# Kernel optimization log

Measured on AMD Instinct MI355X. Metric: run time of the kernel, lower is better.

The kernel has to match this reference:

```python
import jax, jax.numpy as jnp
import numpy as np

N_NODES = 50000
N_EDGES = 800000
IN_CH = 128
HEADS = 4
OUT_CH = 32  # heads * out = in (needed for residual add)


def setup_inputs() -> dict:
    key = jax.random.key(0)
    k1, k2, k3, k4, k5, k6 = jax.random.split(key, 6)
    x = jax.random.normal(k1, (N_NODES, IN_CH), dtype=jnp.float32)
    edge_index = jax.random.randint(k2, (2, N_EDGES), 0, N_NODES, dtype=jnp.int64)
    # GATConv params: lin weight [in, heads*out], attention vectors split src/dst, bias [heads*out]
    W = jax.random.normal(k3, (IN_CH, HEADS * OUT_CH), dtype=jnp.float32) * (1.0 / np.sqrt(IN_CH))
    a_src = jax.random.normal(k4, (HEADS, OUT_CH), dtype=jnp.float32) * 0.1
    a_dst = jax.random.normal(k5, (HEADS, OUT_CH), dtype=jnp.float32) * 0.1
    bias = jax.random.normal(k6, (HEADS * OUT_CH,), dtype=jnp.float32) * 0.01
    return {"x": x, "edge_index": edge_index, "W": W, "a_src": a_src, "a_dst": a_dst, "bias": bias}


def reference(x, edge_index, W, a_src, a_dst, bias):
    N = x.shape[0]
    H, C = a_src.shape
    # PyG GATConv default: add self loops (message flows src -> dst)
    loops = jnp.arange(N, dtype=edge_index.dtype)
    src = jnp.concatenate([edge_index[0], loops])
    dst = jnp.concatenate([edge_index[1], loops])

    h = (x @ W).reshape(N, H, C)                       # [N,H,C]
    alpha_s = jnp.einsum('nhc,hc->nh', h, a_src)       # [N,H]
    alpha_d = jnp.einsum('nhc,hc->nh', h, a_dst)       # [N,H]

    # per-edge logits, LeakyReLU(0.2)
    e = jax.nn.leaky_relu(alpha_s[src] + alpha_d[dst], negative_slope=0.2)  # [E,H]
    # segment softmax over incoming edges of each destination node
    m = jax.ops.segment_max(e, dst, num_segments=N)    # [N,H]
    p = jnp.exp(e - m[dst])
    denom = jax.ops.segment_sum(p, dst, num_segments=N)
    alpha = p / (denom[dst] + 1e-16)                   # [E,H]

    # weighted scatter-sum of source features
    msg = alpha[:, :, None] * h[src]                   # [E,H,C]
    out = jax.ops.segment_sum(msg, dst, num_segments=N)
    out = out.reshape(N, H * C) + bias                 # concat heads + bias

    return jax.nn.elu(out) + x                         # ELU + residual
```

## Files before the change

### kernel.cpp

```cpp
#include <hip/hip_runtime.h>
#include <math.h>


#define CH 128
#define BCOLS 144
#define BKT_SH 8
#define BKT_CAP 8192

typedef short bf16x8 __attribute__((ext_vector_type(8)));
typedef float f32x4 __attribute__((ext_vector_type(4)));

__device__ __forceinline__ short f2bf(float f) {
    unsigned int u = __builtin_bit_cast(unsigned int, f);
    u += 0x7FFFu + ((u >> 16) & 1u);
    return (short)(u >> 16);
}
__device__ __forceinline__ unsigned int cvtpk(float lo, float hi) {
    unsigned int r;
    asm("v_cvt_pk_bf16_f32 %0, %1, %2" : "=v"(r) : "v"(lo), "v"(hi));
    return r;
}
__device__ __forceinline__ float bflo(unsigned int u) {
    return __builtin_bit_cast(float, u << 16);
}
__device__ __forceinline__ float bfhi(unsigned int u) {
    return __builtin_bit_cast(float, u & 0xffff0000u);
}

__global__ void prep(const float* __restrict__ W, const float* __restrict__ a_src,
                     const float* __restrict__ a_dst, short* __restrict__ Wbf,
                     int* __restrict__ gcursor, int nbuk) {
    int i = blockIdx.x * 256 + threadIdx.x;
    if (i < CH * CH) {
        int k = i >> 7, n = i & 127;
        Wbf[n * CH + k] = f2bf(W[i]);
    }
    if (i < 2048) {
        int k = i & 127, idx = i >> 7;
        float sum = 0.f;
        if (idx < 8) {
            int h = idx & 3;
            const float* av = (idx < 4) ? a_src : a_dst;
            #pragma unroll
            for (int c = 0; c < 32; ++c) sum += W[k * CH + h * 32 + c] * av[h * 32 + c];
        }
        Wbf[(CH + idx) * CH + k] = f2bf(sum);
    }
    if (i < nbuk) gcursor[i] = i * BKT_CAP;
}

__device__ __forceinline__ void gemm_body(
    int bid, const float* __restrict__ x, const short* __restrict__ Wbf,
    unsigned short* __restrict__ hb, float* __restrict__ as_, float* __restrict__ ad_,
    int N, short* Wl)
{
    for (int v = threadIdx.x; v < BCOLS * 16; v += 256) {
        int n = v >> 4, k8 = v & 15;
        *(bf16x8*)&Wl[n * CH + ((k8 ^ (n & 7)) << 3)] = *(const bf16x8*)&Wbf[v * 8];
    }
    const int w = threadIdx.x >> 6, l = threadIdx.x & 63;
    const int lr = l & 15, lg = l >> 4;
    const int base = bid * 128 + w * 32;
    __syncthreads();

    bf16x8 afr[2][4];
    #pragma unroll
    for (int mt = 0; mt < 2; ++mt) {
        int arow = base + mt * 16 + lr;
        if (arow >= N) arow = N - 1;
        const float* xr = &x[(size_t)arow * CH + lg * 8];
        #pragma unroll
        for (int ks = 0; ks < 4; ++ks) {
            float4 p0 = *(const float4*)&xr[ks * 32];
            float4 p1 = *(const float4*)&xr[ks * 32 + 4];
            uint4 aw;
            aw.x = cvtpk(p0.x, p0.y); aw.y = cvtpk(p0.z, p0.w);
            aw.z = cvtpk(p1.x, p1.y); aw.w = cvtpk(p1.z, p1.w);
            afr[mt][ks] = __builtin_bit_cast(bf16x8, aw);
        }
    }

    f32x4 acc[2][9];
    #pragma unroll
    for (int mt = 0; mt < 2; ++mt)
        #pragma unroll
        for (int nt = 0; nt < 9; ++nt) acc[mt][nt] = (f32x4){0.f, 0.f, 0.f, 0.f};

    #pragma unroll
    for (int ks = 0; ks < 4; ++ks) {
        #pragma unroll
        for (int nt = 0; nt < 9; ++nt) {
            int col = nt * 16 + lr;
            bf16x8 bfr = *(const bf16x8*)&Wl[col * CH + (((ks * 4 + lg) ^ (col & 7)) << 3)];
            acc[0][nt] = __builtin_amdgcn_mfma_f32_16x16x32_bf16(afr[0][ks], bfr, acc[0][nt], 0, 0, 0);
            acc[1][nt] = __builtin_amdgcn_mfma_f32_16x16x32_bf16(afr[1][ks], bfr, acc[1][nt], 0, 0, 0);
        }
    }

    #pragma unroll
    for (int mt = 0; mt < 2; ++mt) {
        const int rbase = base + mt * 16 + lg * 4;
        #pragma unroll
        for (int nt = 0; nt < 8; ++nt) {
            #pragma unroll
            for (int r = 0; r < 4; r += 2) {
                unsigned int u = cvtpk(acc[mt][nt][r], acc[mt][nt][r + 1]);
                int orow = rbase + r;
                if (orow < N)     hb[(size_t)orow * CH + nt * 16 + lr] = (unsigned short)u;
                if (orow + 1 < N) hb[(size_t)(orow + 1) * CH + nt * 16 + lr] = (unsigned short)(u >> 16);
            }
        }
        #pragma unroll
        for (int r = 0; r < 4; ++r) {
            int orow = rbase + r;
            float val = acc[mt][8][r];
            if (orow < N) {
                if (lr < 4)      as_[orow * 4 + lr] = val;
                else if (lr < 8) ad_[orow * 4 + lr - 4] = val;
            }
        }
    }
}

__device__ __forceinline__ void scatter_body(
    int bid, const int* __restrict__ src, const int* __restrict__ dst,
    int* __restrict__ gcursor, int* __restrict__ ebuf, int E, int N, int NBUK,
    int* lh, int* gbase)
{
    const int t = threadIdx.x;
    for (int j = t; j < NBUK; j += 256) lh[j] = 0;
    __syncthreads();
    const int total = E + N;
    const int base = bid * 1024;
    int pv[4], bk[4], rk[4];
    #pragma unroll
    for (int k = 0; k < 4; ++k) {
        int i = base + k * 256 + t;
        if (i < total) {
            int s, d;
            if (i < E) { s = src[i]; d = dst[i]; }
            else       { s = i - E;  d = s; }
            bk[k] = d >> BKT_SH;
            pv[k] = s | ((d & 255) << 16);
            rk[k] = atomicAdd(&lh[bk[k]], 1);
        } else bk[k] = -1;
    }
    __syncthreads();
    for (int j = t; j < NBUK; j += 256)
        gbase[j] = lh[j] ? atomicAdd(&gcursor[j], lh[j]) : 0;
    __syncthreads();
    #pragma unroll
    for (int k = 0; k < 4; ++k)
        if (bk[k] >= 0) {
            int pos = gbase[bk[k]] + rk[k];
            if (pos < (bk[k] + 1) * BKT_CAP) ebuf[pos] = pv[k];
        }
}

__global__ __launch_bounds__(256) void gemm_scatter(
    const float* __restrict__ x, const short* __restrict__ Wbf,
    unsigned short* __restrict__ hb, float* __restrict__ as_, float* __restrict__ ad_,
    const int* __restrict__ src, const int* __restrict__ dst,
    int* __restrict__ gcursor, int* __restrict__ ebuf,
    int E, int N, int NBUK, int GB)
{
    __shared__ short Wl[BCOLS * CH];
    if ((int)blockIdx.x < GB) {
        gemm_body(blockIdx.x, x, Wbf, hb, as_, ad_, N, Wl);
    } else {
        int* lh = (int*)Wl;
        int* gbase = lh + 256;
        scatter_body(blockIdx.x - GB, src, dst, gcursor, ebuf, E, N, NBUK, lh, gbase);
    }
}

__global__ __launch_bounds__(256) void fine_scatter(
    const int* __restrict__ gcursor, int* __restrict__ ebuf,
    int* __restrict__ row_start, int* __restrict__ row_cnt, int N)
{
    __shared__ int st[BKT_CAP];
    __shared__ int lh[256], lofs[256], lcur[256];
    __shared__ int ws[4];
    const int b = blockIdx.x, t = threadIdx.x;
    const int p0 = b * BKT_CAP;
    int cnt = gcursor[b] - p0; if (cnt > BKT_CAP) cnt = BKT_CAP;
    const int nb = b << BKT_SH;
    lh[t] = 0; lcur[t] = 0;
    __syncthreads();
    for (int e = t; e < cnt; e += 256) {
        int v = ebuf[p0 + e];
        st[e] = v;
        atomicAdd(&lh[v >> 16], 1);
    }
    __syncthreads();
    int v = lh[t], s = v;
    const int lane = t & 63, w = t >> 6;
    #pragma unroll
    for (int off = 1; off < 64; off <<= 1) {
        int u = __shfl_up(s, off, 64);
        if (lane >= off) s += u;
    }
    if (lane == 63) ws[w] = s;
    __syncthreads();
    int wadd = 0;
    if (w > 0) wadd += ws[0];
    if (w > 1) wadd += ws[1];
    if (w > 2) wadd += ws[2];
    int ex = s - v + wadd;
    lofs[t] = ex;
    if (nb + t < N) { row_start[nb + t] = p0 + ex; row_cnt[nb + t] = v; }
    __syncthreads();
    for (int e = t; e < cnt; e += 256) {
        int pv = st[e];
        int ld = pv >> 16;
        int pos = p0 + lofs[ld] + atomicAdd(&lcur[ld], 1);
        ebuf[pos] = pv & 0xFFFF;
    }
}

#define PAIR4(PP, SS, IBASE)                                                    \
    {                                                                           \
        int b0 = 8 * (IBASE) + 4 * half;                                        \
        int b1 = b0 + 8, b2 = b0 + 16, b3 = b0 + 24;                            \
        float pb0 = __shfl((PP), b0 + h2, 64);                                  \
        float pb1 = __shfl((PP), b1 + h2, 64);                                  \
        float pb2 = __shfl((PP), b2 + h2, 64);                                  \
        float pb3 = __shfl((PP), b3 + h2, 64);                                  \
        int sb0 = __shfl((SS), b0, 64);                                         \
        int sb1 = __shfl((SS), b1, 64);                                         \
        int sb2 = __shfl((SS), b2, 64);                                         \
        int sb3 = __shfl((SS), b3, 64);                                         \
        uint2 hv0 = *(const uint2*)&hb[(size_t)sb0 * CH + l31 * 4];             \
        uint2 hv1 = *(const uint2*)&hb[(size_t)sb1 * CH + l31 * 4];             \
        uint2 hv2 = *(const uint2*)&hb[(size_t)sb2 * CH + l31 * 4];             \
        uint2 hv3 = *(const uint2*)&hb[(size_t)sb3 * CH + l31 * 4];             \
        acc0 = fmaf(pb0, bflo(hv0.x), acc0); acc1 = fmaf(pb0, bfhi(hv0.x), acc1); \
        acc2 = fmaf(pb0, bflo(hv0.y), acc2); acc3 = fmaf(pb0, bfhi(hv0.y), acc3); \
        acc0 = fmaf(pb1, bflo(hv1.x), acc0); acc1 = fmaf(pb1, bfhi(hv1.x), acc1); \
        acc2 = fmaf(pb1, bflo(hv1.y), acc2); acc3 = fmaf(pb1, bfhi(hv1.y), acc3); \
        acc0 = fmaf(pb2, bflo(hv2.x), acc0); acc1 = fmaf(pb2, bfhi(hv2.x), acc1); \
        acc2 = fmaf(pb2, bflo(hv2.y), acc2); acc3 = fmaf(pb2, bfhi(hv2.y), acc3); \
        acc0 = fmaf(pb3, bflo(hv3.x), acc0); acc1 = fmaf(pb3, bfhi(hv3.x), acc1); \
        acc2 = fmaf(pb3, bflo(hv3.y), acc2); acc3 = fmaf(pb3, bfhi(hv3.y), acc3); \
    }

#define PAIR1(PP, SS, IBASE)                                                    \
    {                                                                           \
        int b0 = 8 * (IBASE) + 4 * half;                                        \
        float pb0 = __shfl((PP), b0 + h2, 64);                                  \
        int   sb0 = __shfl((SS), b0, 64);                                       \
        uint2 hv0 = *(const uint2*)&hb[(size_t)sb0 * CH + l31 * 4];             \
        acc0 = fmaf(pb0, bflo(hv0.x), acc0); acc1 = fmaf(pb0, bfhi(hv0.x), acc1); \
        acc2 = fmaf(pb0, bflo(hv0.y), acc2); acc3 = fmaf(pb0, bfhi(hv0.y), acc3); \
    }

__global__ __launch_bounds__(256) void gat_aggregate(
    const unsigned short* __restrict__ hb, const float* __restrict__ as_,
    const float* __restrict__ ad_, const int* __restrict__ row_start,
    const int* __restrict__ row_cnt, const int* __restrict__ esrc,
    const float* __restrict__ bias, const float* __restrict__ x,
    float* __restrict__ out, int N)
{
    int wid = blockIdx.x * 4 + (threadIdx.x >> 6);
    int lane = threadIdx.x & 63;
    if (wid >= N) return;
    const int l31 = lane & 31;
    const int half = lane >> 5;
    const int hq = lane & 3;
    const int eslot = lane >> 2;
    const int h2 = l31 >> 3;
    const float adv = ad_[wid * 4 + hq];
    const int jb = row_start[wid];
    const int je = jb + row_cnt[wid];

    float denp = 0.f;
    float acc0 = 0.f, acc1 = 0.f, acc2 = 0.f, acc3 = 0.f;
    for (int j0 = jb; j0 < je; j0 += 32) {
        int ei0 = j0 + eslot, ei1 = j0 + 16 + eslot;
        int s0 = 0, s1 = 0; float p0 = 0.f, p1 = 0.f;
        if (ei0 < je) {
            s0 = esrc[ei0];
            float e = as_[s0 * 4 + hq] + adv;
            e = fmaxf(e, 0.2f * e);
            p0 = __expf(e);
        }
        if (ei1 < je) {
            s1 = esrc[ei1];
            float e = as_[s1 * 4 + hq] + adv;
            e = fmaxf(e, 0.2f * e);
            p1 = __expf(e);
        }
        denp += p0 + p1;
        int rem = je - j0; if (rem > 32) rem = 32;
        int npair = (rem + 1) >> 1;
        int npA = npair < 8 ? npair : 8;
        int i = 0;
        for (; i + 3 < npA; i += 4) PAIR4(p0, s0, i);
        for (; i < npA; ++i)        PAIR1(p0, s0, i);
        if (npair > 8) {
            int npB = npair - 8;
            i = 0;
            for (; i + 3 < npB; i += 4) PAIR4(p1, s1, i);
            for (; i < npB; ++i)        PAIR1(p1, s1, i);
        }
    }
    #pragma unroll
    for (int m = 4; m < 64; m <<= 1) denp += __shfl_xor(denp, m, 64);
    float den = __shfl(denp, h2, 64);
    acc0 += __shfl_xor(acc0, 32, 64);
    acc1 += __shfl_xor(acc1, 32, 64);
    acc2 += __shfl_xor(acc2, 32, 64);
    acc3 += __shfl_xor(acc3, 32, 64);
    if (half == 0) {
        float inv = 1.f / (den + 1e-16f);
        float4 bv = *(const float4*)&bias[l31 * 4];
        float4 xv = *(const float4*)&x[(size_t)wid * CH + l31 * 4];
        float o0 = acc0 * inv + bv.x;
        float o1 = acc1 * inv + bv.y;
        float o2 = acc2 * inv + bv.z;
        float o3 = acc3 * inv + bv.w;
        o0 = (o0 > 0.f) ? o0 : expm1f(o0);
        o1 = (o1 > 0.f) ? o1 : expm1f(o1);
        o2 = (o2 > 0.f) ? o2 : expm1f(o2);
        o3 = (o3 > 0.f) ? o3 : expm1f(o3);
        float4 ov = make_float4(o0 + xv.x, o1 + xv.y, o2 + xv.z, o3 + xv.w);
        *(float4*)&out[(size_t)wid * CH + l31 * 4] = ov;
    }
}

extern "C" void kernel_launch(void* const* d_in, const int* in_sizes, int n_in,
                              void* d_out, int out_size, void* d_ws, size_t ws_size,
                              hipStream_t stream) {
    const float* x     = (const float*)d_in[0];
    const int*   ei    = (const int*)d_in[1];
    const float* W     = (const float*)d_in[2];
    const float* a_src = (const float*)d_in[3];
    const float* a_dst = (const float*)d_in[4];
    const float* bias  = (const float*)d_in[5];
    float* out = (float*)d_out;

    const int N = in_sizes[0] / CH;
    const int E = in_sizes[1] / 2;
    const int* src = ei;
    const int* dst = ei + E;
    const int total = E + N;
    const int NBUK = (N + 255) >> BKT_SH;

    unsigned short* hb = (unsigned short*)d_ws;
    float* as_ = (float*)(hb + (size_t)N * CH);
    float* ad_ = as_ + (size_t)N * 4;
    short* Wbf = (short*)(ad_ + (size_t)N * 4);
    int* row_start = (int*)(Wbf + BCOLS * CH);
    int* row_cnt   = row_start + N;
    int* gcursor   = row_cnt + N;
    int* ebuf      = gcursor + 256;

    const int GB = (N + 127) / 128;
    const int SB = (total + 1023) / 1024;

    prep<<<64, 256, 0, stream>>>(W, a_src, a_dst, Wbf, gcursor, NBUK);
    gemm_scatter<<<GB + SB, 256, 0, stream>>>(x, Wbf, hb, as_, ad_,
                                              src, dst, gcursor, ebuf,
                                              E, N, NBUK, GB);
    fine_scatter<<<NBUK, 256, 0, stream>>>(gcursor, ebuf, row_start, row_cnt, N);
    gat_aggregate<<<(N + 3) / 4, 256, 0, stream>>>(hb, as_, ad_, row_start, row_cnt, ebuf, bias, x, out, N);
}
```

Baseline: 161.9 us.

## Fuse fine bucket sort into aggregation with 32-node buckets sorted in LDS

Shrinks the coarse scatter buckets from 256 to 32 destination nodes and removes the separate fine_scatter kernel. The aggregation kernel now loads each bucket, sorts it by destination in shared memory, and then has each wave aggregate 8 nodes, reading source ids from LDS instead of global ebuf. This drops a kernel launch, the global row_start/row_cnt arrays and a round trip of ebuf through memory. In exchange there are many more atomic buckets (about 1563) in the coarse scatter, and the bucket capacity of 768 could overflow for high-degree clusters, which would drop edges.

```diff
diff --git a/kernel.cpp b/kernel.cpp
--- a/kernel.cpp
+++ b/kernel.cpp
@@ -4,8 +4,10 @@
 
 #define CH 128
 #define BCOLS 144
-#define BKT_SH 8
-#define BKT_CAP 8192
+#define BKT_SH 5
+#define BKT_NODES 32
+#define BKT_CAP 768
+#define NBUK_PAD 1600
 
 typedef short bf16x8 __attribute__((ext_vector_type(8)));
 typedef float f32x4 __attribute__((ext_vector_type(4)));
@@ -141,7 +143,7 @@
             if (i < E) { s = src[i]; d = dst[i]; }
             else       { s = i - E;  d = s; }
             bk[k] = d >> BKT_SH;
-            pv[k] = s | ((d & 255) << 16);
+            pv[k] = s | ((d & (BKT_NODES - 1)) << 16);
             rk[k] = atomicAdd(&lh[bk[k]], 1);
         } else bk[k] = -1;
     }
@@ -169,52 +171,8 @@
         gemm_body(blockIdx.x, x, Wbf, hb, as_, ad_, N, Wl);
     } else {
         int* lh = (int*)Wl;
-        int* gbase = lh + 256;
+        int* gbase = lh + NBUK_PAD;
         scatter_body(blockIdx.x - GB, src, dst, gcursor, ebuf, E, N, NBUK, lh, gbase);
-    }
-}
-
-__global__ __launch_bounds__(256) void fine_scatter(
-    const int* __restrict__ gcursor, int* __restrict__ ebuf,
-    int* __restrict__ row_start, int* __restrict__ row_cnt, int N)
-{
-    __shared__ int st[BKT_CAP];
-    __shared__ int lh[256], lofs[256], lcur[256];
-    __shared__ int ws[4];
-    const int b = blockIdx.x, t = threadIdx.x;
-    const int p0 = b * BKT_CAP;
-    int cnt = gcursor[b] - p0; if (cnt > BKT_CAP) cnt = BKT_CAP;
-    const int nb = b << BKT_SH;
-    lh[t] = 0; lcur[t] = 0;
-    __syncthreads();
-    for (int e = t; e < cnt; e += 256) {
-        int v = ebuf[p0 + e];
-        st[e] = v;
-        atomicAdd(&lh[v >> 16], 1);
-    }
-    __syncthreads();
-    int v = lh[t], s = v;
-    const int lane = t & 63, w = t >> 6;
-    #pragma unroll
-    for (int off = 1; off < 64; off <<= 1) {
-        int u = __shfl_up(s, off, 64);
-        if (lane >= off) s += u;
-    }
-    if (lane == 63) ws[w] = s;
-    __syncthreads();
-    int wadd = 0;
-    if (w > 0) wadd += ws[0];
-    if (w > 1) wadd += ws[1];
-    if (w > 2) wadd += ws[2];
-    int ex = s - v + wadd;
-    lofs[t] = ex;
-    if (nb + t < N) { row_start[nb + t] = p0 + ex; row_cnt[nb + t] = v; }
-    __syncthreads();
-    for (int e = t; e < cnt; e += 256) {
-        int pv = st[e];
-        int ld = pv >> 16;
-        int pos = p0 + lofs[ld] + atomicAdd(&lcur[ld], 1);
-        ebuf[pos] = pv & 0xFFFF;
     }
 }
 
@@ -254,77 +212,113 @@
         acc2 = fmaf(pb0, bflo(hv0.y), acc2); acc3 = fmaf(pb0, bfhi(hv0.y), acc3); \
     }
 
-__global__ __launch_bounds__(256) void gat_aggregate(
+__global__ __launch_bounds__(256) void csr_aggregate(
+    const int* __restrict__ gcursor, const int* __restrict__ ebuf,
     const unsigned short* __restrict__ hb, const float* __restrict__ as_,
-    const float* __restrict__ ad_, const int* __restrict__ row_start,
-    const int* __restrict__ row_cnt, const int* __restrict__ esrc,
-    const float* __restrict__ bias, const float* __restrict__ x,
-    float* __restrict__ out, int N)
+    const float* __restrict__ ad_, const float* __restrict__ bias,
+    const float* __restrict__ x, float* __restrict__ out, int N)
 {
-    int wid = blockIdx.x * 4 + (threadIdx.x >> 6);
-    int lane = threadIdx.x & 63;
-    if (wid >= N) return;
+    __shared__ int st[BKT_CAP];
+    __shared__ unsigned short st2[BKT_CAP];
+    __shared__ int lh[BKT_NODES], lofs[BKT_NODES], lcur[BKT_NODES];
+    const int b = blockIdx.x, t = threadIdx.x;
+    const int p0 = b * BKT_CAP;
+    int cnt = gcursor[b] - p0; if (cnt > BKT_CAP) cnt = BKT_CAP;
+    if (t < BKT_NODES) { lh[t] = 0; lcur[t] = 0; }
+    __syncthreads();
+    for (int e = t; e < cnt; e += 256) {
+        int v = ebuf[p0 + e];
+        st[e] = v;
+        atomicAdd(&lh[v >> 16], 1);
+    }
+    __syncthreads();
+    if (t < 64) {
+        int v = (t < BKT_NODES) ? lh[t] : 0;
+        int s = v;
+        #pragma unroll
+        for (int off = 1; off < 32; off <<= 1) {
+            int u = __shfl_up(s, off, 64);
+            if (t >= off) s += u;
+        }
+        if (t < BKT_NODES) lofs[t] = s - v;
+    }
+    __syncthreads();
+    for (int e = t; e < cnt; e += 256) {
+        int v = st[e];
+        int pos = lofs[v >> 16] + atomicAdd(&lcur[v >> 16], 1);
+        st2[pos] = (unsigned short)(v & 0xFFFF);
+    }
+    __syncthreads();
+
+    const int wv = t >> 6, lane = t & 63;
     const int l31 = lane & 31;
     const int half = lane >> 5;
     const int hq = lane & 3;
     const int eslot = lane >> 2;
     const int h2 = l31 >> 3;
-    const float adv = ad_[wid * 4 + hq];
-    const int jb = row_start[wid];
-    const int je = jb + row_cnt[wid];
-
-    float denp = 0.f;
-    float acc0 = 0.f, acc1 = 0.f, acc2 = 0.f, acc3 = 0.f;
-    for (int j0 = jb; j0 < je; j0 += 32) {
-        int ei0 = j0 + eslot, ei1 = j0 + 16 + eslot;
-        int s0 = 0, s1 = 0; float p0 = 0.f, p1 = 0.f;
-        if (ei0 < je) {
-            s0 = esrc[ei0];
-            float e = as_[s0 * 4 + hq] + adv;
-            e = fmaxf(e, 0.2f * e);
-            p0 = __expf(e);
-        }
-        if (ei1 < je) {
-            s1 = esrc[ei1];
-            float e = as_[s1 * 4 + hq] + adv;
-            e = fmaxf(e, 0.2f * e);
-            p1 = __expf(e);
-        }
-        denp += p0 + p1;
-        int rem = je - j0; if (rem > 32) rem = 32;
-        int npair = (rem + 1) >> 1;
-        int npA = npair < 8 ? npair : 8;
-        int i = 0;
-        for (; i + 3 < npA; i += 4) PAIR4(p0, s0, i);
-        for (; i < npA; ++i)        PAIR1(p0, s0, i);
-        if (npair > 8) {
-            int npB = npair - 8;
-            i = 0;
-            for (; i + 3 < npB; i += 4) PAIR4(p1, s1, i);
-            for (; i < npB; ++i)        PAIR1(p1, s1, i);
-        }
-    }
-    #pragma unroll
-    for (int m = 4; m < 64; m <<= 1) denp += __shfl_xor(denp, m, 64);
-    float den = __shfl(denp, h2, 64);
-    acc0 += __shfl_xor(acc0, 32, 64);
-    acc1 += __shfl_xor(acc1, 32, 64);
-    acc2 += __shfl_xor(acc2, 32, 64);
-    acc3 += __shfl_xor(acc3, 32, 64);
-    if (half == 0) {
-        float inv = 1.f / (den + 1e-16f);
-        float4 bv = *(const float4*)&bias[l31 * 4];
-        float4 xv = *(const float4*)&x[(size_t)wid * CH + l31 * 4];
-        float o0 = acc0 * inv + bv.x;
-        float o1 = acc1 * inv + bv.y;
-        float o2 = acc2 * inv + bv.z;
-        float o3 = acc3 * inv + bv.w;
-        o0 = (o0 > 0.f) ? o0 : expm1f(o0);
-        o1 = (o1 > 0.f) ? o1 : expm1f(o1);
-        o2 = (o2 > 0.f) ? o2 : expm1f(o2);
-        o3 = (o3 > 0.f) ? o3 : expm1f(o3);
-        float4 ov = make_float4(o0 + xv.x, o1 + xv.y, o2 + xv.z, o3 + xv.w);
-        *(float4*)&out[(size_t)wid * CH + l31 * 4] = ov;
+    const int nb = b << BKT_SH;
+
+    for (int k = 0; k < 8; ++k) {
+        const int ln = wv * 8 + k;
+        const int n = nb + ln;
+        if (n >= N) continue;
+        const float adv = ad_[n * 4 + hq];
+        const int jb = lofs[ln];
+        const int je = jb + lh[ln];
+
+        float denp = 0.f;
+        float acc0 = 0.f, acc1 = 0.f, acc2 = 0.f, acc3 = 0.f;
+        for (int j0 = jb; j0 < je; j0 += 32) {
+            int ei0 = j0 + eslot, ei1 = j0 + 16 + eslot;
+            int s0 = 0, s1 = 0; float p0v = 0.f, p1v = 0.f;
+            if (ei0 < je) {
+                s0 = st2[ei0];
+                float e = as_[s0 * 4 + hq] + adv;
+                e = fmaxf(e, 0.2f * e);
+                p0v = __expf(e);
+            }
+            if (ei1 < je) {
+                s1 = st2[ei1];
+                float e = as_[s1 * 4 + hq] + adv;
+                e = fmaxf(e, 0.2f * e);
+                p1v = __expf(e);
+            }
+            denp += p0v + p1v;
+            int rem = je - j0; if (rem > 32) rem = 32;
+            int npair = (rem + 1) >> 1;
+            int npA = npair < 8 ? npair : 8;
+            int i = 0;
+            for (; i + 3 < npA; i += 4) PAIR4(p0v, s0, i);
+            for (; i < npA; ++i)        PAIR1(p0v, s0, i);
+            if (npair > 8) {
+                int npB = npair - 8;
+                i = 0;
+                for (; i + 3 < npB; i += 4) PAIR4(p1v, s1, i);
+                for (; i < npB; ++i)        PAIR1(p1v, s1, i);
+            }
+        }
+        #pragma unroll
+        for (int m = 4; m < 64; m <<= 1) denp += __shfl_xor(denp, m, 64);
+        float den = __shfl(denp, h2, 64);
+        acc0 += __shfl_xor(acc0, 32, 64);
+        acc1 += __shfl_xor(acc1, 32, 64);
+        acc2 += __shfl_xor(acc2, 32, 64);
+        acc3 += __shfl_xor(acc3, 32, 64);
+        if (half == 0) {
+            float inv = 1.f / (den + 1e-16f);
+            float4 bv = *(const float4*)&bias[l31 * 4];
+            float4 xv = *(const float4*)&x[(size_t)n * CH + l31 * 4];
+            float o0 = acc0 * inv + bv.x;
+            float o1 = acc1 * inv + bv.y;
+            float o2 = acc2 * inv + bv.z;
+            float o3 = acc3 * inv + bv.w;
+            o0 = (o0 > 0.f) ? o0 : expm1f(o0);
+            o1 = (o1 > 0.f) ? o1 : expm1f(o1);
+            o2 = (o2 > 0.f) ? o2 : expm1f(o2);
+            o3 = (o3 > 0.f) ? o3 : expm1f(o3);
+            float4 ov = make_float4(o0 + xv.x, o1 + xv.y, o2 + xv.z, o3 + xv.w);
+            *(float4*)&out[(size_t)n * CH + l31 * 4] = ov;
+        }
     }
 }
 
@@ -344,16 +338,14 @@
     const int* src = ei;
     const int* dst = ei + E;
     const int total = E + N;
-    const int NBUK = (N + 255) >> BKT_SH;
+    const int NBUK = (N + BKT_NODES - 1) >> BKT_SH;
 
     unsigned short* hb = (unsigned short*)d_ws;
     float* as_ = (float*)(hb + (size_t)N * CH);
     float* ad_ = as_ + (size_t)N * 4;
     short* Wbf = (short*)(ad_ + (size_t)N * 4);
-    int* row_start = (int*)(Wbf + BCOLS * CH);
-    int* row_cnt   = row_start + N;
-    int* gcursor   = row_cnt + N;
-    int* ebuf      = gcursor + 256;
+    int* gcursor   = (int*)(Wbf + BCOLS * CH);
+    int* ebuf      = gcursor + 2048;
 
     const int GB = (N + 127) / 128;
     const int SB = (total + 1023) / 1024;
@@ -362,6 +354,5 @@
     gemm_scatter<<<GB + SB, 256, 0, stream>>>(x, Wbf, hb, as_, ad_,
                                               src, dst, gcursor, ebuf,
                                               E, N, NBUK, GB);
-    fine_scatter<<<NBUK, 256, 0, stream>>>(gcursor, ebuf, row_start, row_cnt, N);
-    gat_aggregate<<<(N + 3) / 4, 256, 0, stream>>>(hb, as_, ad_, row_start, row_cnt, ebuf, bias, x, out, N);
-}
+    csr_aggregate<<<NBUK, 256, 0, stream>>>(gcursor, ebuf, hb, as_, ad_, bias, x, out, N);
+}
```

After: 160.5 us. About the same (-0.9%).
